# Optimization experiments

Hardware: AMD Instinct MI355X
Metric: run time of the kernel (lower is better)

The kernel has to match this reference:

```python
import jax, jax.numpy as jnp
import numpy as np

V, E, H, L, B, S = 32000, 512, 512, 2, 8, 512


def setup_inputs() -> dict:
    key = jax.random.key(0)
    ks = jax.random.split(key, 16)
    emb = jax.random.normal(ks[0], (V, E), jnp.float32) * 0.02
    emb = emb.at[0].set(0.0)  # padding_idx=0
    init_state = jax.random.normal(ks[1], (2, L, H), jnp.float32)  # [h;c] params
    def xav(k, shp):
        fan_in, fan_out = shp[1], shp[0]
        lim = np.sqrt(6.0 / (fan_in + fan_out)).astype(np.float32)
        return jax.random.uniform(k, shp, jnp.float32, -lim, lim)
    inp = {
        'emb_table': emb,
        'init_state': init_state,
        'w_ih0': xav(ks[2], (4 * H, E)), 'w_hh0': xav(ks[3], (4 * H, H)),
        'b_ih0': jnp.zeros((4 * H,), jnp.float32), 'b_hh0': jnp.zeros((4 * H,), jnp.float32),
        'w_ih1': xav(ks[4], (4 * H, H)), 'w_hh1': xav(ks[5], (4 * H, H)),
        'b_ih1': jnp.zeros((4 * H,), jnp.float32), 'b_hh1': jnp.zeros((4 * H,), jnp.float32),
        'wg': xav(ks[6], (2 * H, H)), 'bg': jnp.zeros((2 * H,), jnp.float32),
        'wd': xav(ks[7], (V, H)), 'bd': jnp.zeros((V,), jnp.float32),
        'eps': jax.random.normal(ks[8], (B, S, H), jnp.float32),
        'x': jax.random.randint(ks[9], (B, S), 0, V, jnp.int64),
    }
    return inp


def _lstm_layer(xs, h0, c0, w_ih, w_hh, b_ih, b_hh):
    # xs: [S, B, in]; returns hidden sequence [S, B, H]
    b = b_ih + b_hh
    def step(carry, x_t):
        h, c = carry
        gates = x_t @ w_ih.T + h @ w_hh.T + b  # [B, 4H]
        i, f, g, o = jnp.split(gates, 4, axis=-1)  # torch gate order i,f,g,o
        c = jax.nn.sigmoid(f) * c + jax.nn.sigmoid(i) * jnp.tanh(g)
        h = jax.nn.sigmoid(o) * jnp.tanh(c)
        return (h, c), h
    _, hs = jax.lax.scan(step, (h0, c0), xs)
    return hs


def reference(emb_table, init_state, w_ih0, w_hh0, b_ih0, b_hh0,
              w_ih1, w_hh1, b_ih1, b_hh1, wg, bg, wd, bd, eps, x):
    Bsz = x.shape[0]
    embedding = emb_table[x]  # [B, S, E]
    h0 = jnp.broadcast_to(init_state[0][:, None, :], (L, Bsz, H))
    c0 = jnp.broadcast_to(init_state[1][:, None, :], (L, Bsz, H))
    xs = embedding.transpose(1, 0, 2)  # time-major [S, B, E]
    hs0 = _lstm_layer(xs, h0[0], c0[0], w_ih0, w_hh0, b_ih0, b_hh0)
    hs1 = _lstm_layer(hs0, h0[1], c0[1], w_ih1, w_hh1, b_ih1, b_hh1)
    out = hs1.transpose(1, 0, 2)  # [B, S, H]
    stats = out @ wg.T + bg  # [B, S, 2H]
    std = jax.nn.softplus(stats[:, :, :H])  # diagonal of covariance matrix
    mu = stats[:, :, H:]
    # MultivariateNormal(mu, cov=diag(std)).rsample() => mu + sqrt(std) * eps
    sample = mu + jnp.sqrt(std) * eps
    logits = sample @ wd.T + bd  # [B, S, V]
    return (logits, mu, std)
```

## Files before the change

kernel.cpp:

```cpp
#include <hip/hip_runtime.h>


typedef __attribute__((ext_vector_type(4))) float f32x4;
typedef __attribute__((ext_vector_type(8))) short short8;
typedef __attribute__((ext_vector_type(4))) unsigned short u16x4;

#define V_SZ 32000
#define E_SZ 512
#define H_SZ 512
#define B_SZ 8
#define S_SZ 512
#define NTOK 4096
#define G4H  2048

__device__ __forceinline__ unsigned short f2bf(float x) {
  unsigned int b = __float_as_uint(x);
  b += 0x7FFFu + ((b >> 16) & 1u);
  return (unsigned short)(b >> 16);
}
__device__ __forceinline__ float bf2f(unsigned short u) {
  return __uint_as_float(((unsigned int)u) << 16);
}

__device__ __forceinline__ void split4(const f32x4 v, u16x4& hv, u16x4& lv) {
  unsigned short h0 = f2bf(v.x); lv.x = f2bf(v.x - bf2f(h0)); hv.x = h0;
  unsigned short h1 = f2bf(v.y); lv.y = f2bf(v.y - bf2f(h1)); hv.y = h1;
  unsigned short h2 = f2bf(v.z); lv.z = f2bf(v.z - bf2f(h2)); hv.z = h2;
  unsigned short h3 = f2bf(v.w); lv.w = f2bf(v.w - bf2f(h3)); hv.w = h3;
}

__global__ void split_kernel(const float* __restrict__ src,
                             unsigned short* __restrict__ hi,
                             unsigned short* __restrict__ lo, int n4) {
  int i = blockIdx.x * 256 + threadIdx.x;
  if (i >= n4) return;
  f32x4 v = ((const f32x4*)src)[i];
  u16x4 hv, lv;
  split4(v, hv, lv);
  ((u16x4*)hi)[i] = hv;
  ((u16x4*)lo)[i] = lv;
}

__global__ void bias_sum_kernel(const float* __restrict__ a0, const float* __restrict__ c0,
                                const float* __restrict__ a1, const float* __restrict__ c1,
                                float* __restrict__ o0, float* __restrict__ o1) {
  int i = blockIdx.x * 256 + threadIdx.x;
  if (i < G4H) { o0[i] = a0[i] + c0[i]; o1[i] = a1[i] + c1[i]; }
}

__global__ void embed_split_kernel(const float* __restrict__ emb, const int* __restrict__ x,
                                   unsigned short* __restrict__ hi, unsigned short* __restrict__ lo) {
  int gid = blockIdx.x * 256 + threadIdx.x;
  int r = gid >> 7;
  int kq = (gid & 127) << 2;
  int tok = x[r];
  f32x4 v = *(const f32x4*)(emb + (size_t)tok * E_SZ + kq);
  u16x4 hv, lv;
  split4(v, hv, lv);
  *(u16x4*)(hi + (size_t)r * E_SZ + kq) = hv;
  *(u16x4*)(lo + (size_t)r * E_SZ + kq) = lv;
}

__device__ __forceinline__ int swz32(int row, int seg) {
  return row * 32 + (((seg ^ (row & 3)) << 3));
}

__global__ __launch_bounds__(256, 2) void gemm3_kernel(
    const unsigned short* __restrict__ Ah, const unsigned short* __restrict__ Al,
    const unsigned short* __restrict__ Bh, const unsigned short* __restrict__ Bl,
    const float* __restrict__ bias, float* __restrict__ C,
    int M, int N, int K) {
  __shared__ unsigned short sAh[128 * 32];
  __shared__ unsigned short sAl[128 * 32];
  __shared__ unsigned short sBh[128 * 32];
  __shared__ unsigned short sBl[128 * 32];

  const int t = threadIdx.x;
  const int lane = t & 63;
  const int wave = t >> 6;
  const int wr = wave >> 1, wc = wave & 1;
  const size_t m0 = (size_t)blockIdx.y * 128;
  const size_t n0 = (size_t)blockIdx.x * 128;

  f32x4 acc[4][4];
#pragma unroll
  for (int i = 0; i < 4; ++i)
#pragma unroll
    for (int j = 0; j < 4; ++j) acc[i][j] = (f32x4){0.f, 0.f, 0.f, 0.f};

  const int r0 = t >> 2;
  const int seg0 = t & 3;

  const int nk = K >> 5;
  for (int ks = 0; ks < nk; ++ks) {
    const int k0 = ks << 5;
    short8 vAh[2], vAl[2], vBh[2], vBl[2];
#pragma unroll
    for (int r = 0; r < 2; ++r) {
      int row = r0 + r * 64;
      size_t ga = (m0 + row) * (size_t)K + k0 + seg0 * 8;
      size_t gb = (n0 + row) * (size_t)K + k0 + seg0 * 8;
      vAh[r] = *(const short8*)(Ah + ga);
      vAl[r] = *(const short8*)(Al + ga);
      vBh[r] = *(const short8*)(Bh + gb);
      vBl[r] = *(const short8*)(Bl + gb);
    }
    __syncthreads();
#pragma unroll
    for (int r = 0; r < 2; ++r) {
      int row = r0 + r * 64;
      int d = swz32(row, seg0);
      *(short8*)(sAh + d) = vAh[r];
      *(short8*)(sAl + d) = vAl[r];
      *(short8*)(sBh + d) = vBh[r];
      *(short8*)(sBl + d) = vBl[r];
    }
    __syncthreads();

    short8 ah[4], al[4], bh[4], bl[4];
    const int seg = lane >> 4;
#pragma unroll
    for (int m = 0; m < 4; ++m) {
      int row = wr * 64 + m * 16 + (lane & 15);
      int d = swz32(row, seg);
      ah[m] = *(const short8*)(sAh + d);
      al[m] = *(const short8*)(sAl + d);
    }
#pragma unroll
    for (int n = 0; n < 4; ++n) {
      int row = wc * 64 + n * 16 + (lane & 15);
      int d = swz32(row, seg);
      bh[n] = *(const short8*)(sBh + d);
      bl[n] = *(const short8*)(sBl + d);
    }
#pragma unroll
    for (int m = 0; m < 4; ++m) {
#pragma unroll
      for (int n = 0; n < 4; ++n) {
        acc[m][n] = __builtin_amdgcn_mfma_f32_16x16x32_bf16(ah[m], bh[n], acc[m][n], 0, 0, 0);
        acc[m][n] = __builtin_amdgcn_mfma_f32_16x16x32_bf16(ah[m], bl[n], acc[m][n], 0, 0, 0);
        acc[m][n] = __builtin_amdgcn_mfma_f32_16x16x32_bf16(al[m], bh[n], acc[m][n], 0, 0, 0);
      }
    }
  }

#pragma unroll
  for (int m = 0; m < 4; ++m) {
#pragma unroll
    for (int n = 0; n < 4; ++n) {
      size_t gr0 = m0 + wr * 64 + m * 16 + ((lane >> 4) << 2);
      size_t gc = n0 + wc * 64 + n * 16 + (lane & 15);
      float bv = bias ? bias[gc] : 0.f;
#pragma unroll
      for (int j = 0; j < 4; ++j) {
        C[(gr0 + j) * (size_t)N + gc] = acc[m][n][j] + bv;
      }
    }
  }
}

#define SEQ_NB 192

__device__ __forceinline__ float sigm(float x) { return 1.f / (1.f + expf(-x)); }

__global__ __launch_bounds__(256, 1) void lstm_seq_kernel(
    const float* __restrict__ gx0,
    const float* __restrict__ w_hh0,
    const float* __restrict__ w_ih1,
    const float* __restrict__ w_hh1,
    const float* __restrict__ b1s,
    const float* __restrict__ initst,
    float* __restrict__ h0_all,
    float* __restrict__ h1_all,
    float* __restrict__ gx1,
    unsigned short* __restrict__ hs1h,
    unsigned short* __restrict__ hs1l,
    unsigned int* __restrict__ sig0,
    unsigned int* __restrict__ sig1,
    unsigned int* __restrict__ sig1a) {
  const int blk = blockIdx.x;
  const int t = threadIdx.x;
  const int grp = blk >> 6;
  const int lb = blk & 63;

  __shared__ float hA[8][512];
  __shared__ float gates_s[32][8];

  const int tb = t >> 7;
  const int rg = (t >> 4) & 7;
  const int kg = t & 15;

  const float* wsrc = (grp == 0) ? w_hh0 : (grp == 1) ? w_ih1 : w_hh1;
  f32x4 w[4][8];
#pragma unroll
  for (int rr = 0; rr < 4; ++rr) {
    int rl = rg * 4 + rr;
    int grow = (rl >> 3) * H_SZ + lb * 8 + (rl & 7);
    const float* src = wsrc + (size_t)grow * H_SZ + kg * 4;
#pragma unroll
    for (int j = 0; j < 8; ++j) w[rr][j] = *(const f32x4*)(src + j * 64);
  }

  const int cu = t >> 3, cb = t & 7;
  const int cunit = lb * 8 + cu;
  float creg = 0.f;
  float bgi = 0.f, bgf = 0.f, bgg = 0.f, bgo = 0.f;
  if (t < 64) {
    if (grp == 0) creg = initst[1024 + cunit];
    if (grp == 2) {
      creg = initst[1024 + 512 + cunit];
      bgi = b1s[cunit];
      bgf = b1s[512 + cunit];
      bgg = b1s[1024 + cunit];
      bgo = b1s[1536 + cunit];
    }
  }

  for (int step = 0; step < 512; ++step) {
    float pgi = 0.f, pgf = 0.f, pgg = 0.f, pgo = 0.f;
    if (grp == 0 && t < 64) {
      const float* gx = gx0 + ((size_t)(cb * S_SZ + step)) * G4H + cunit;
      pgi = gx[0];
      pgf = gx[512];
      pgg = gx[1024];
      pgo = gx[1536];
    }

    if (t < 64) {
      if (grp == 0) {
        if (step > 0) {
          const unsigned int* s0 = sig0 + (size_t)(step - 1) * 64;
          while (true) {
            unsigned int v = __hip_atomic_load(&s0[t], __ATOMIC_RELAXED, __HIP_MEMORY_SCOPE_AGENT);
            if (__all(v != 0)) break;
            __builtin_amdgcn_s_sleep(1);
          }
        }
      } else if (grp == 1) {
        const unsigned int* s0 = sig0 + (size_t)step * 64;
        while (true) {
          unsigned int v = __hip_atomic_load(&s0[t], __ATOMIC_RELAXED, __HIP_MEMORY_SCOPE_AGENT);
          if (__all(v != 0)) break;
          __builtin_amdgcn_s_sleep(1);
        }
      } else {
        const unsigned int* sa = sig1a + (size_t)step * 64 + lb;
        const unsigned int* s1 = (step > 0) ? (sig1 + (size_t)(step - 1) * 64) : nullptr;
        while (true) {
          int ok = (__hip_atomic_load(sa, __ATOMIC_RELAXED, __HIP_MEMORY_SCOPE_AGENT) != 0);
          if (s1) ok &= (__hip_atomic_load(&s1[t], __ATOMIC_RELAXED, __HIP_MEMORY_SCOPE_AGENT) != 0);
          if (__all(ok)) break;
          __builtin_amdgcn_s_sleep(1);
        }
      }
    }
    __syncthreads();

    float gxv[4];
    if (grp == 2 && t < 64) {
      const float* gp = gx1 + ((size_t)step * 64 + lb) * 256;
#pragma unroll
      for (int g = 0; g < 4; ++g) gxv[g] = gp[(g * 8 + cu) * 8 + cb];
    }

    {
      const float* src;
      if (grp == 0)       src = (step == 0) ? nullptr : (h0_all + (size_t)(step - 1) * 4096);
      else if (grp == 1)  src = h0_all + (size_t)step * 4096;
      else                src = (step == 0) ? nullptr : (h1_all + (size_t)(step - 1) * 4096);
      if (src) {
#pragma unroll
        for (int i = 0; i < 4; ++i) {
          int idx = t + i * 256;
          int b = idx >> 7;
          int kc = (idx & 127) << 2;
          *(f32x4*)&hA[b][kc] = *(const f32x4*)(src + b * H_SZ + kc);
        }
      } else {
        const float* ini = initst + (grp == 0 ? 0 : 512);
#pragma unroll
        for (int i = 0; i < 4; ++i) {
          int idx = t + i * 256;
          int b = idx >> 7;
          int kc = (idx & 127) << 2;
          *(f32x4*)&hA[b][kc] = *(const f32x4*)(ini + kc);
        }
      }
    }
    __syncthreads();

    float acc[4][4];
#pragma unroll
    for (int rr = 0; rr < 4; ++rr)
#pragma unroll
      for (int bq = 0; bq < 4; ++bq) acc[rr][bq] = 0.f;
#pragma unroll
    for (int bq = 0; bq < 4; ++bq) {
      const float* hb = &hA[tb * 4 + bq][0];
#pragma unroll
      for (int j = 0; j < 8; ++j) {
        f32x4 hq = *(const f32x4*)(hb + kg * 4 + j * 64);
#pragma unroll
        for (int rr = 0; rr < 4; ++rr)
          acc[rr][bq] += w[rr][j].x * hq.x + w[rr][j].y * hq.y +
                         w[rr][j].z * hq.z + w[rr][j].w * hq.w;
      }
    }
#pragma unroll
    for (int s = 1; s < 16; s <<= 1) {
#pragma unroll
      for (int rr = 0; rr < 4; ++rr)
#pragma unroll
        for (int bq = 0; bq < 4; ++bq)
          acc[rr][bq] += __shfl_xor(acc[rr][bq], s, 64);
    }

    if (grp == 1) {
      if (kg == 0) {
        unsigned long long* gq =
            (unsigned long long*)(gx1 + ((size_t)step * 64 + lb) * 256);
#pragma unroll
        for (int rr = 0; rr < 4; ++rr) {
          int rl = rg * 4 + rr;
          unsigned long long lo =
              ((unsigned long long)__float_as_uint(acc[rr][1]) << 32) |
              (unsigned long long)__float_as_uint(acc[rr][0]);
          unsigned long long hi =
              ((unsigned long long)__float_as_uint(acc[rr][3]) << 32) |
              (unsigned long long)__float_as_uint(acc[rr][2]);
          __hip_atomic_store(&gq[rl * 4 + tb * 2], lo, __ATOMIC_RELAXED, __HIP_MEMORY_SCOPE_AGENT);
          __hip_atomic_store(&gq[rl * 4 + tb * 2 + 1], hi, __ATOMIC_RELAXED, __HIP_MEMORY_SCOPE_AGENT);
        }
      }
      __syncthreads();
      if (t == 0)
        __hip_atomic_store(&sig1a[(size_t)step * 64 + lb], 1u,
                           __ATOMIC_RELAXED, __HIP_MEMORY_SCOPE_AGENT);
    } else {
      if (kg == 0) {
#pragma unroll
        for (int rr = 0; rr < 4; ++rr)
#pragma unroll
          for (int bq = 0; bq < 4; ++bq)
            gates_s[rg * 4 + rr][tb * 4 + bq] = acc[rr][bq];
      }
      __syncthreads();

      if (t < 64) {
        float gi, gf, gg, go;
        if (grp == 0) {
          gi = gates_s[cu][cb] + pgi;
          gf = gates_s[8 + cu][cb] + pgf;
          gg = gates_s[16 + cu][cb] + pgg;
          go = gates_s[24 + cu][cb] + pgo;
        } else {
          gi = gates_s[cu][cb] + gxv[0] + bgi;
          gf = gates_s[8 + cu][cb] + gxv[1] + bgf;
          gg = gates_s[16 + cu][cb] + gxv[2] + bgg;
          go = gates_s[24 + cu][cb] + gxv[3] + bgo;
        }
        float cn = sigm(gf) * creg + sigm(gi) * tanhf(gg);
        float h = sigm(go) * tanhf(cn);
        creg = cn;
        if (grp == 0) {
          __hip_atomic_store(&h0_all[(size_t)step * 4096 + cb * H_SZ + cunit], h,
                             __ATOMIC_RELAXED, __HIP_MEMORY_SCOPE_AGENT);
        } else {
          __hip_atomic_store(&h1_all[(size_t)step * 4096 + cb * H_SZ + cunit], h,
                             __ATOMIC_RELAXED, __HIP_MEMORY_SCOPE_AGENT);
          size_t r = (size_t)(cb * S_SZ + step) * H_SZ + cunit;
          unsigned short hh = f2bf(h);
          hs1h[r] = hh;
          hs1l[r] = f2bf(h - bf2f(hh));
        }
      }
      if (t == 0) {
        asm volatile("s_waitcnt vmcnt(0)" ::: "memory");
        unsigned int* slot = (grp == 0) ? (sig0 + (size_t)step * 64 + lb)
                                        : (sig1 + (size_t)step * 64 + lb);
        __hip_atomic_store(slot, 1u, __ATOMIC_RELAXED, __HIP_MEMORY_SCOPE_AGENT);
      }
    }
  }
}

__global__ void sample_kernel(const float* __restrict__ stats, const float* __restrict__ eps,
                              unsigned short* __restrict__ sh, unsigned short* __restrict__ sl,
                              float* __restrict__ omu, float* __restrict__ ostd) {
  int gid = blockIdx.x * 256 + threadIdx.x;
  int r = gid >> 9, hh = gid & 511;
  float sp = stats[(size_t)r * 1024 + hh];
  float mu = stats[(size_t)r * 1024 + 512 + hh];
  float sd = (sp > 20.f) ? sp : log1pf(expf(sp));
  float smp = mu + sqrtf(sd) * eps[gid];
  omu[gid] = mu;
  ostd[gid] = sd;
  unsigned short h = f2bf(smp);
  sh[gid] = h;
  sl[gid] = f2bf(smp - bf2f(h));
}

extern "C" void kernel_launch(void* const* d_in, const int* in_sizes, int n_in,
                              void* d_out, int out_size, void* d_ws, size_t ws_size,
                              hipStream_t stream) {
  const float* emb    = (const float*)d_in[0];
  const float* initst = (const float*)d_in[1];
  const float* w_ih0  = (const float*)d_in[2];
  const float* w_hh0  = (const float*)d_in[3];
  const float* b_ih0  = (const float*)d_in[4];
  const float* b_hh0  = (const float*)d_in[5];
  const float* w_ih1  = (const float*)d_in[6];
  const float* w_hh1  = (const float*)d_in[7];
  const float* b_ih1  = (const float*)d_in[8];
  const float* b_hh1  = (const float*)d_in[9];
  const float* wg     = (const float*)d_in[10];
  const float* bg     = (const float*)d_in[11];
  const float* wd     = (const float*)d_in[12];
  const float* bd     = (const float*)d_in[13];
  const float* eps    = (const float*)d_in[14];
  const int*   x      = (const int*)d_in[15];

  char* ws = (char*)d_ws;
  size_t off = 0;
  auto alloc = [&](size_t sz) {
    void* p = ws + off;
    off = (off + sz + 255) & ~(size_t)255;
    return p;
  };
  unsigned int* sig0     = (unsigned int*)alloc((size_t)512 * 64 * 4);
  unsigned int* sig1     = (unsigned int*)alloc((size_t)512 * 64 * 4);
  unsigned int* sig1a    = (unsigned int*)alloc((size_t)512 * 64 * 4);
  float* b0s             = (float*)alloc(G4H * 4);
  float* b1s             = (float*)alloc(G4H * 4);
  unsigned short* wih0h  = (unsigned short*)alloc((size_t)G4H * E_SZ * 2);
  unsigned short* wih0l  = (unsigned short*)alloc((size_t)G4H * E_SZ * 2);
  unsigned short* wgh    = (unsigned short*)alloc((size_t)1024 * H_SZ * 2);
  unsigned short* wgl    = (unsigned short*)alloc((size_t)1024 * H_SZ * 2);
  unsigned short* wdh    = (unsigned short*)alloc((size_t)V_SZ * H_SZ * 2);
  unsigned short* wdl    = (unsigned short*)alloc((size_t)V_SZ * H_SZ * 2);
  unsigned short* a0h    = (unsigned short*)alloc((size_t)NTOK * E_SZ * 2);
  unsigned short* a0l    = (unsigned short*)alloc((size_t)NTOK * E_SZ * 2);
  float* gx0             = (float*)alloc((size_t)NTOK * G4H * 4);
  float* gx1             = (float*)alloc((size_t)512 * 64 * 256 * 4);
  float* h0_all          = (float*)alloc((size_t)512 * 4096 * 4);
  float* h1_all          = (float*)alloc((size_t)512 * 4096 * 4);
  unsigned short* hs1h   = (unsigned short*)alloc((size_t)NTOK * H_SZ * 2);
  unsigned short* hs1l   = (unsigned short*)alloc((size_t)NTOK * H_SZ * 2);
  float* stats           = (float*)alloc((size_t)NTOK * 1024 * 4);
  unsigned short* smph   = (unsigned short*)alloc((size_t)NTOK * H_SZ * 2);
  unsigned short* smpl   = (unsigned short*)alloc((size_t)NTOK * H_SZ * 2);

  float* out_logits = (float*)d_out;
  float* out_mu     = out_logits + (size_t)NTOK * V_SZ;
  float* out_std    = out_mu + (size_t)NTOK * H_SZ;

  (void)hipMemsetAsync(sig0, 0, (size_t)512 * 64 * 4, stream);
  (void)hipMemsetAsync(sig1, 0, (size_t)512 * 64 * 4, stream);
  (void)hipMemsetAsync(sig1a, 0, (size_t)512 * 64 * 4, stream);

  split_kernel<<<(G4H * E_SZ / 4 + 255) / 256, 256, 0, stream>>>(w_ih0, wih0h, wih0l, G4H * E_SZ / 4);
  split_kernel<<<(1024 * H_SZ / 4 + 255) / 256, 256, 0, stream>>>(wg, wgh, wgl, 1024 * H_SZ / 4);
  split_kernel<<<(V_SZ * H_SZ / 4 + 255) / 256, 256, 0, stream>>>(wd, wdh, wdl, V_SZ * H_SZ / 4);
  bias_sum_kernel<<<8, 256, 0, stream>>>(b_ih0, b_hh0, b_ih1, b_hh1, b0s, b1s);

  embed_split_kernel<<<NTOK * 128 / 256, 256, 0, stream>>>(emb, x, a0h, a0l);

  gemm3_kernel<<<dim3(G4H / 128, NTOK / 128), 256, 0, stream>>>(
      a0h, a0l, wih0h, wih0l, b0s, gx0, NTOK, G4H, E_SZ);

  lstm_seq_kernel<<<SEQ_NB, 256, 0, stream>>>(
      gx0, w_hh0, w_ih1, w_hh1, b1s, initst, h0_all, h1_all, gx1,
      hs1h, hs1l, sig0, sig1, sig1a);

  gemm3_kernel<<<dim3(1024 / 128, NTOK / 128), 256, 0, stream>>>(
      hs1h, hs1l, wgh, wgl, bg, stats, NTOK, 1024, H_SZ);

  sample_kernel<<<NTOK * H_SZ / 256, 256, 0, stream>>>(stats, eps, smph, smpl, out_mu, out_std);

  gemm3_kernel<<<dim3(V_SZ / 128, NTOK / 128), 256, 0, stream>>>(
      smph, smpl, wdh, wdl, bd, out_logits, NTOK, V_SZ, H_SZ);
}
```

Before: 4.185 ms.

## Replace per-block flag arrays with atomic step counters polled per wave

Inter-block step signalling in the persistent LSTM kernel changes from 64 per-block flags per step to one atomic counter per step, incremented with fetch_add. Every wave now polls the counter itself, with lane 0 loading it and readfirstlane broadcasting the value, so the block-wide barrier after the wait is gone. Hidden-state stores are packed into 64-bit pairs through a lane shuffle. The aim is to shorten the critical-path latency of each recurrent step, at the cost of contended atomics on one address and more waves polling global memory.

Measured after the change: 4.790 ms. 1.14x slower.

```diff
diff --git a/kernel.cpp b/kernel.cpp
--- a/kernel.cpp
+++ b/kernel.cpp
@@ -175,13 +175,14 @@
     float* __restrict__ gx1,
     unsigned short* __restrict__ hs1h,
     unsigned short* __restrict__ hs1l,
-    unsigned int* __restrict__ sig0,
-    unsigned int* __restrict__ sig1,
+    unsigned int* __restrict__ cnt0,
+    unsigned int* __restrict__ cnt1,
     unsigned int* __restrict__ sig1a) {
   const int blk = blockIdx.x;
   const int t = threadIdx.x;
   const int grp = blk >> 6;
   const int lb = blk & 63;
+  const int lane = t & 63;
 
   __shared__ float hA[8][512];
   __shared__ float gates_s[32][8];
@@ -226,35 +227,43 @@
       pgo = gx[1536];
     }
 
-    if (t < 64) {
-      if (grp == 0) {
-        if (step > 0) {
-          const unsigned int* s0 = sig0 + (size_t)(step - 1) * 64;
-          while (true) {
-            unsigned int v = __hip_atomic_load(&s0[t], __ATOMIC_RELAXED, __HIP_MEMORY_SCOPE_AGENT);
-            if (__all(v != 0)) break;
-            __builtin_amdgcn_s_sleep(1);
-          }
-        }
-      } else if (grp == 1) {
-        const unsigned int* s0 = sig0 + (size_t)step * 64;
+    if (grp == 0) {
+      if (step > 0) {
+        const unsigned int* c = &cnt0[step - 1];
         while (true) {
-          unsigned int v = __hip_atomic_load(&s0[t], __ATOMIC_RELAXED, __HIP_MEMORY_SCOPE_AGENT);
-          if (__all(v != 0)) break;
+          unsigned int v = 0;
+          if (lane == 0)
+            v = __hip_atomic_load(c, __ATOMIC_RELAXED, __HIP_MEMORY_SCOPE_AGENT);
+          v = (unsigned int)__builtin_amdgcn_readfirstlane((int)v);
+          if (v >= 64u) break;
           __builtin_amdgcn_s_sleep(1);
         }
-      } else {
-        const unsigned int* sa = sig1a + (size_t)step * 64 + lb;
-        const unsigned int* s1 = (step > 0) ? (sig1 + (size_t)(step - 1) * 64) : nullptr;
-        while (true) {
-          int ok = (__hip_atomic_load(sa, __ATOMIC_RELAXED, __HIP_MEMORY_SCOPE_AGENT) != 0);
-          if (s1) ok &= (__hip_atomic_load(&s1[t], __ATOMIC_RELAXED, __HIP_MEMORY_SCOPE_AGENT) != 0);
-          if (__all(ok)) break;
-          __builtin_amdgcn_s_sleep(1);
-        }
-      }
-    }
-    __syncthreads();
+      }
+    } else if (grp == 1) {
+      const unsigned int* c = &cnt0[step];
+      while (true) {
+        unsigned int v = 0;
+        if (lane == 0)
+          v = __hip_atomic_load(c, __ATOMIC_RELAXED, __HIP_MEMORY_SCOPE_AGENT);
+        v = (unsigned int)__builtin_amdgcn_readfirstlane((int)v);
+        if (v >= 64u) break;
+        __builtin_amdgcn_s_sleep(1);
+      }
+    } else {
+      const unsigned int* fa = sig1a + (size_t)step * 64 + lb;
+      const unsigned int* c1 = (step > 0) ? (cnt1 + step - 1) : nullptr;
+      while (true) {
+        unsigned int a = 1, b = 64;
+        if (lane == 0) {
+          a = __hip_atomic_load(fa, __ATOMIC_RELAXED, __HIP_MEMORY_SCOPE_AGENT);
+          if (c1) b = __hip_atomic_load(c1, __ATOMIC_RELAXED, __HIP_MEMORY_SCOPE_AGENT);
+        }
+        a = (unsigned int)__builtin_amdgcn_readfirstlane((int)a);
+        b = (unsigned int)__builtin_amdgcn_readfirstlane((int)b);
+        if (a != 0u && b >= 64u) break;
+        __builtin_amdgcn_s_sleep(1);
+      }
+    }
 
     float gxv[4];
     if (grp == 2 && t < 64) {
@@ -333,9 +342,11 @@
         }
       }
       __syncthreads();
-      if (t == 0)
+      if (t == 0) {
+        asm volatile("s_waitcnt vmcnt(0)" ::: "memory");
         __hip_atomic_store(&sig1a[(size_t)step * 64 + lb], 1u,
                            __ATOMIC_RELAXED, __HIP_MEMORY_SCOPE_AGENT);
+      }
     } else {
       if (kg == 0) {
 #pragma unroll
@@ -362,12 +373,17 @@
         float cn = sigm(gf) * creg + sigm(gi) * tanhf(gg);
         float h = sigm(go) * tanhf(cn);
         creg = cn;
-        if (grp == 0) {
-          __hip_atomic_store(&h0_all[(size_t)step * 4096 + cb * H_SZ + cunit], h,
-                             __ATOMIC_RELAXED, __HIP_MEMORY_SCOPE_AGENT);
-        } else {
-          __hip_atomic_store(&h1_all[(size_t)step * 4096 + cb * H_SZ + cunit], h,
-                             __ATOMIC_RELAXED, __HIP_MEMORY_SCOPE_AGENT);
+        float hp = __shfl_xor(h, 8, 64);
+        float* hbase = (grp == 0) ? h0_all : h1_all;
+        if ((t & 8) == 0) {
+          unsigned long long pk =
+              ((unsigned long long)__float_as_uint(hp) << 32) |
+              (unsigned long long)__float_as_uint(h);
+          unsigned long long* dst = (unsigned long long*)
+              (hbase + (size_t)step * 4096 + cb * H_SZ + cunit);
+          __hip_atomic_store(dst, pk, __ATOMIC_RELAXED, __HIP_MEMORY_SCOPE_AGENT);
+        }
+        if (grp == 2) {
           size_t r = (size_t)(cb * S_SZ + step) * H_SZ + cunit;
           unsigned short hh = f2bf(h);
           hs1h[r] = hh;
@@ -376,9 +392,8 @@
       }
       if (t == 0) {
         asm volatile("s_waitcnt vmcnt(0)" ::: "memory");
-        unsigned int* slot = (grp == 0) ? (sig0 + (size_t)step * 64 + lb)
-                                        : (sig1 + (size_t)step * 64 + lb);
-        __hip_atomic_store(slot, 1u, __ATOMIC_RELAXED, __HIP_MEMORY_SCOPE_AGENT);
+        unsigned int* c = (grp == 0) ? (cnt0 + step) : (cnt1 + step);
+        __hip_atomic_fetch_add(c, 1u, __ATOMIC_RELAXED, __HIP_MEMORY_SCOPE_AGENT);
       }
     }
   }
@@ -427,8 +442,8 @@
     off = (off + sz + 255) & ~(size_t)255;
     return p;
   };
-  unsigned int* sig0     = (unsigned int*)alloc((size_t)512 * 64 * 4);
-  unsigned int* sig1     = (unsigned int*)alloc((size_t)512 * 64 * 4);
+  unsigned int* cnt0     = (unsigned int*)alloc(512 * 4);
+  unsigned int* cnt1     = (unsigned int*)alloc(512 * 4);
   unsigned int* sig1a    = (unsigned int*)alloc((size_t)512 * 64 * 4);
   float* b0s             = (float*)alloc(G4H * 4);
   float* b1s             = (float*)alloc(G4H * 4);
@@ -454,8 +469,8 @@
   float* out_mu     = out_logits + (size_t)NTOK * V_SZ;
   float* out_std    = out_mu + (size_t)NTOK * H_SZ;
 
-  (void)hipMemsetAsync(sig0, 0, (size_t)512 * 64 * 4, stream);
-  (void)hipMemsetAsync(sig1, 0, (size_t)512 * 64 * 4, stream);
+  (void)hipMemsetAsync(cnt0, 0, 512 * 4, stream);
+  (void)hipMemsetAsync(cnt1, 0, 512 * 4, stream);
   (void)hipMemsetAsync(sig1a, 0, (size_t)512 * 64 * 4, stream);
 
   split_kernel<<<(G4H * E_SZ / 4 + 255) / 256, 256, 0, stream>>>(w_ih0, wih0h, wih0l, G4H * E_SZ / 4);
@@ -470,7 +485,7 @@
 
   lstm_seq_kernel<<<SEQ_NB, 256, 0, stream>>>(
       gx0, w_hh0, w_ih1, w_hh1, b1s, initst, h0_all, h1_all, gx1,
-      hs1h, hs1l, sig0, sig1, sig1a);
+      hs1h, hs1l, cnt0, cnt1, sig1a);
 
   gemm3_kernel<<<dim3(1024 / 128, NTOK / 128), 256, 0, stream>>>(
       hs1h, hs1l, wgh, wgl, bg, stats, NTOK, 1024, H_SZ);
```
